# Kernel optimization log

Hardware: AMD Instinct MI355X
Metric: run time of the kernel (lower is better)

Reference implementation:

```python
import jax, jax.numpy as jnp
import numpy as np

B, N, K, D, H = 8, 128, 64, 256, 8  # batch, groups, keys-per-query, k_dim (=h_size), n_head


def setup_inputs() -> dict:
    key = jax.random.key(0)
    kq, kk, kv, kw, kb = jax.random.split(key, 5)
    bound = 1.0 / np.sqrt(D)  # torch nn.Bilinear default init bound
    return {
        "q": jax.random.normal(kq, (B, N, 1, D), jnp.float32),
        "k": jax.random.normal(kk, (B, N, K, D), jnp.float32),
        "v": jax.random.normal(kv, (B, N, K, D), jnp.float32),
        "W": jax.random.uniform(kw, (H, D, D), jnp.float32, -bound, bound),
        "b": jax.random.uniform(kb, (H,), jnp.float32, -bound, bound),
    }


def reference(q, k, v, W, b):
    Bs, Ns, Ks, Ds = k.shape
    Hh = W.shape[0]
    qe = q[:, :, 0, :]  # (B,N,D); torch expands q over K, einsum broadcasts instead
    # nn.Bilinear: scores[b,n,k,h] = q[b,n,:] @ W[h] @ k[b,n,k,:] + b[h]
    scores = jnp.einsum('bnd,hde,bnke->bnkh', qe, W, k) + b  # (B,N,K,H)
    # Faithful to torch's .view(B, N, -1, K): row-major reinterpretation of the
    # trailing (K, H) pair as (H, K) — a dim-mixing reshape, not a transpose.
    attn = scores.reshape(Bs, Ns, Hh, Ks)
    attn = jax.nn.softmax(attn, axis=-1)  # softmax over last dim (dropout p=0)
    # matmul(attn, v) -> (B,N,H,Dv); then sum over the head axis
    output = jnp.einsum('bnhk,bnkd->bnd', attn, v)
    return output, attn
```

## Files before the change

### kernel.cpp

```cpp
#include <hip/hip_runtime.h>
#include <math.h>

namespace {

constexpr int D  = 256;
constexpr int H  = 8;

__global__ __launch_bounds__(256) void qw_kernel(
    const float* __restrict__ q, const float* __restrict__ W,
    float* __restrict__ qW) {
  __shared__ float qT[256][20];
  const int tid = threadIdx.x;
  const int bn0 = blockIdx.x * 16;
  const int h   = blockIdx.y;
  for (int i = 0; i < 16; ++i)
    qT[tid][i] = q[(size_t)(bn0 + i) * D + tid];
  __syncthreads();

  const int r0 = (tid >> 6) << 2;
  const int e0 = (tid & 63) << 2;
  float acc[4][4];
  #pragma unroll
  for (int r = 0; r < 4; ++r)
    #pragma unroll
    for (int e = 0; e < 4; ++e) acc[r][e] = 0.f;

  const float4* W4 = reinterpret_cast<const float4*>(W + (size_t)h * D * D);
  const int ecol = e0 >> 2;
  for (int d = 0; d < D; ++d) {
    float4 qv = *reinterpret_cast<const float4*>(&qT[d][r0]);
    float4 wv = W4[d * 64 + ecol];
    const float qa[4] = {qv.x, qv.y, qv.z, qv.w};
    const float wa[4] = {wv.x, wv.y, wv.z, wv.w};
    #pragma unroll
    for (int r = 0; r < 4; ++r)
      #pragma unroll
      for (int e = 0; e < 4; ++e)
        acc[r][e] += qa[r] * wa[e];
  }
  #pragma unroll
  for (int r = 0; r < 4; ++r) {
    float4 o = make_float4(acc[r][0], acc[r][1], acc[r][2], acc[r][3]);
    *reinterpret_cast<float4*>(&qW[(size_t)(bn0 + r0 + r) * (H * D) + h * D + e0]) = o;
  }
}

__global__ __launch_bounds__(256, 4) void attn_kernel(
    const float* __restrict__ qW, const float* __restrict__ kin,
    const float* __restrict__ vin, const float* __restrict__ bin,
    float* __restrict__ out, float* __restrict__ attn_out) {
  __shared__ float qW_lds[H][260];
  __shared__ float s_lds[512];
  __shared__ float wpart[4][64];
  __shared__ float s_red[4][260];
  const int tid = threadIdx.x;
  const int bn  = blockIdx.x;
  const int wid = tid >> 6;
  const int ln  = tid & 63;

  const float4* v4p = reinterpret_cast<const float4*>(vin) + (size_t)bn * 4096;
  float4 vb0[8];
  #pragma unroll
  for (int j = 0; j < 8; ++j) vb0[j] = v4p[(wid * 16 + j) * 64 + ln];

  const float4* qw4 = reinterpret_cast<const float4*>(qW) + (size_t)bn * 512;
  {
    float4 q0 = qw4[tid];
    float4 q1 = qw4[tid + 256];
    *reinterpret_cast<float4*>(&qW_lds[tid >> 6][(tid & 63) << 2]) = q0;
    *reinterpret_cast<float4*>(&qW_lds[(tid + 256) >> 6][(tid & 63) << 2]) = q1;
  }
  __syncthreads();

  {
    const int krow = tid >> 2;
    const int hp   = tid & 3;
    const float4* k4  = reinterpret_cast<const float4*>(kin) + (size_t)bn * 4096 + krow * 64;
    const float4* a04 = reinterpret_cast<const float4*>(&qW_lds[hp][0]);
    const float4* a14 = reinterpret_cast<const float4*>(&qW_lds[hp + 4][0]);
    float acc0 = bin[hp], acc1 = bin[hp + 4];
    for (int blk = 0; blk < 8; ++blk) {
      float4 kb[8];
      #pragma unroll
      for (int j = 0; j < 8; ++j) kb[j] = k4[blk * 8 + j];
      #pragma unroll
      for (int j = 0; j < 8; ++j) {
        float4 a0 = a04[blk * 8 + j];
        float4 a1 = a14[blk * 8 + j];
        acc0 += a0.x * kb[j].x + a0.y * kb[j].y + a0.z * kb[j].z + a0.w * kb[j].w;
        acc1 += a1.x * kb[j].x + a1.y * kb[j].y + a1.z * kb[j].z + a1.w * kb[j].w;
      }
    }
    s_lds[krow * 8 + hp]     = acc0;
    s_lds[krow * 8 + hp + 4] = acc1;
  }
  __syncthreads();

  float4 vb1[8];
  #pragma unroll
  for (int j = 0; j < 8; ++j) vb1[j] = v4p[(wid * 16 + 8 + j) * 64 + ln];

  {
    float wp = 0.f;
    #pragma unroll
    for (int i = 0; i < 2; ++i) {
      const int c = wid * 2 + i;
      float x = s_lds[c * 64 + ln];
      float m = x;
      #pragma unroll
      for (int off = 32; off; off >>= 1) m = fmaxf(m, __shfl_xor(m, off, 64));
      float e = expf(x - m);
      float s = e;
      #pragma unroll
      for (int off = 32; off; off >>= 1) s += __shfl_xor(s, off, 64);
      float a = e / s;
      attn_out[(size_t)bn * 512 + c * 64 + ln] = a;
      wp += a;
    }
    wpart[wid][ln] = wp;
  }
  __syncthreads();

  {
    float4 acc = make_float4(0.f, 0.f, 0.f, 0.f);
    #pragma unroll
    for (int j = 0; j < 8; ++j) {
      const int kr = wid * 16 + j;
      float w = wpart[0][kr] + wpart[1][kr] + wpart[2][kr] + wpart[3][kr];
      acc.x += w * vb0[j].x; acc.y += w * vb0[j].y;
      acc.z += w * vb0[j].z; acc.w += w * vb0[j].w;
    }
    #pragma unroll
    for (int j = 0; j < 8; ++j) {
      const int kr = wid * 16 + 8 + j;
      float w = wpart[0][kr] + wpart[1][kr] + wpart[2][kr] + wpart[3][kr];
      acc.x += w * vb1[j].x; acc.y += w * vb1[j].y;
      acc.z += w * vb1[j].z; acc.w += w * vb1[j].w;
    }
    *reinterpret_cast<float4*>(&s_red[wid][ln << 2]) = acc;
  }
  __syncthreads();

  out[(size_t)bn * D + tid] =
      s_red[0][tid] + s_red[1][tid] + s_red[2][tid] + s_red[3][tid];
}

}

extern "C" void kernel_launch(void* const* d_in, const int* in_sizes, int n_in,
                              void* d_out, int out_size, void* d_ws, size_t ws_size,
                              hipStream_t stream) {
  const float* q = (const float*)d_in[0];
  const float* k = (const float*)d_in[1];
  const float* v = (const float*)d_in[2];
  const float* W = (const float*)d_in[3];
  const float* b = (const float*)d_in[4];

  float* out  = (float*)d_out;
  float* attn = out + 262144;
  float* qWbuf = (float*)d_ws;

  hipLaunchKernelGGL(qw_kernel, dim3(64, 8), dim3(256), 0, stream, q, W, qWbuf);
  hipLaunchKernelGGL(attn_kernel, dim3(1024), dim3(256), 0, stream, qWbuf, k, v, b, out, attn);
}
```

Baseline: 49.01 us.

## Split fused attention kernel into score/softmax and PV kernels with 2x grid

Replaces the single fused attention kernel with two kernels. The first computes scores and softmax for half of the key rows per block over a 1024x2 grid. The second reads attn back from global memory and computes the weighted sum of v over a 1024x2 grid split by half of D. This exposes more blocks and lowers register pressure (launch bounds go to 8 blocks per SM). The cost is an extra kernel launch, a round trip of attn through global memory, and each score block reloading qW.

```diff
diff --git a/kernel.cpp b/kernel.cpp
--- a/kernel.cpp
+++ b/kernel.cpp
@@ -45,23 +45,16 @@
   }
 }
 
-__global__ __launch_bounds__(256, 4) void attn_kernel(
+__global__ __launch_bounds__(256, 8) void score_kernel(
     const float* __restrict__ qW, const float* __restrict__ kin,
-    const float* __restrict__ vin, const float* __restrict__ bin,
-    float* __restrict__ out, float* __restrict__ attn_out) {
+    const float* __restrict__ bin, float* __restrict__ attn_out) {
   __shared__ float qW_lds[H][260];
-  __shared__ float s_lds[512];
-  __shared__ float wpart[4][64];
-  __shared__ float s_red[4][260];
+  __shared__ float s_lds[256];
   const int tid = threadIdx.x;
   const int bn  = blockIdx.x;
+  const int kh  = blockIdx.y;
   const int wid = tid >> 6;
   const int ln  = tid & 63;
-
-  const float4* v4p = reinterpret_cast<const float4*>(vin) + (size_t)bn * 4096;
-  float4 vb0[8];
-  #pragma unroll
-  for (int j = 0; j < 8; ++j) vb0[j] = v4p[(wid * 16 + j) * 64 + ln];
 
   const float4* qw4 = reinterpret_cast<const float4*>(qW) + (size_t)bn * 512;
   {
@@ -73,76 +66,83 @@
   __syncthreads();
 
   {
-    const int krow = tid >> 2;
-    const int hp   = tid & 3;
-    const float4* k4  = reinterpret_cast<const float4*>(kin) + (size_t)bn * 4096 + krow * 64;
-    const float4* a04 = reinterpret_cast<const float4*>(&qW_lds[hp][0]);
-    const float4* a14 = reinterpret_cast<const float4*>(&qW_lds[hp + 4][0]);
-    float acc0 = bin[hp], acc1 = bin[hp + 4];
+    const int krl = tid >> 3;
+    const int h   = tid & 7;
+    const float4* k4 = reinterpret_cast<const float4*>(kin) +
+                       (size_t)bn * 4096 + (size_t)(kh * 32 + krl) * 64;
+    const float4* a4 = reinterpret_cast<const float4*>(&qW_lds[h][0]);
+    float acc = bin[h];
     for (int blk = 0; blk < 8; ++blk) {
       float4 kb[8];
       #pragma unroll
       for (int j = 0; j < 8; ++j) kb[j] = k4[blk * 8 + j];
       #pragma unroll
       for (int j = 0; j < 8; ++j) {
-        float4 a0 = a04[blk * 8 + j];
-        float4 a1 = a14[blk * 8 + j];
-        acc0 += a0.x * kb[j].x + a0.y * kb[j].y + a0.z * kb[j].z + a0.w * kb[j].w;
-        acc1 += a1.x * kb[j].x + a1.y * kb[j].y + a1.z * kb[j].z + a1.w * kb[j].w;
+        float4 a = a4[blk * 8 + j];
+        acc += a.x * kb[j].x + a.y * kb[j].y + a.z * kb[j].z + a.w * kb[j].w;
       }
     }
-    s_lds[krow * 8 + hp]     = acc0;
-    s_lds[krow * 8 + hp + 4] = acc1;
-  }
-  __syncthreads();
-
-  float4 vb1[8];
-  #pragma unroll
-  for (int j = 0; j < 8; ++j) vb1[j] = v4p[(wid * 16 + 8 + j) * 64 + ln];
-
-  {
-    float wp = 0.f;
-    #pragma unroll
-    for (int i = 0; i < 2; ++i) {
-      const int c = wid * 2 + i;
-      float x = s_lds[c * 64 + ln];
-      float m = x;
-      #pragma unroll
-      for (int off = 32; off; off >>= 1) m = fmaxf(m, __shfl_xor(m, off, 64));
-      float e = expf(x - m);
-      float s = e;
-      #pragma unroll
-      for (int off = 32; off; off >>= 1) s += __shfl_xor(s, off, 64);
-      float a = e / s;
-      attn_out[(size_t)bn * 512 + c * 64 + ln] = a;
-      wp += a;
-    }
-    wpart[wid][ln] = wp;
+    s_lds[krl * 8 + h] = acc;
   }
   __syncthreads();
 
   {
-    float4 acc = make_float4(0.f, 0.f, 0.f, 0.f);
+    float x = s_lds[wid * 64 + ln];
+    float m = x;
     #pragma unroll
-    for (int j = 0; j < 8; ++j) {
-      const int kr = wid * 16 + j;
-      float w = wpart[0][kr] + wpart[1][kr] + wpart[2][kr] + wpart[3][kr];
-      acc.x += w * vb0[j].x; acc.y += w * vb0[j].y;
-      acc.z += w * vb0[j].z; acc.w += w * vb0[j].w;
-    }
+    for (int off = 32; off; off >>= 1) m = fmaxf(m, __shfl_xor(m, off, 64));
+    float e = expf(x - m);
+    float s = e;
     #pragma unroll
-    for (int j = 0; j < 8; ++j) {
-      const int kr = wid * 16 + 8 + j;
-      float w = wpart[0][kr] + wpart[1][kr] + wpart[2][kr] + wpart[3][kr];
-      acc.x += w * vb1[j].x; acc.y += w * vb1[j].y;
-      acc.z += w * vb1[j].z; acc.w += w * vb1[j].w;
-    }
-    *reinterpret_cast<float4*>(&s_red[wid][ln << 2]) = acc;
+    for (int off = 32; off; off >>= 1) s += __shfl_xor(s, off, 64);
+    attn_out[(size_t)bn * 512 + (4 * kh + wid) * 64 + ln] = e / s;
+  }
+}
+
+__global__ __launch_bounds__(256, 8) void pv_kernel(
+    const float* __restrict__ vin, const float* __restrict__ attn_in,
+    float* __restrict__ out) {
+  __shared__ float ws[64];
+  __shared__ float s_red[8][32][4];
+  const int tid = threadIdx.x;
+  const int bn  = blockIdx.x;
+  const int dh  = blockIdx.y;
+
+  if (tid < 64) {
+    const float* ap = attn_in + (size_t)bn * 512 + tid;
+    float w = 0.f;
+    #pragma unroll
+    for (int c = 0; c < 8; ++c) w += ap[c * 64];
+    ws[tid] = w;
   }
   __syncthreads();
 
-  out[(size_t)bn * D + tid] =
-      s_red[0][tid] + s_red[1][tid] + s_red[2][tid] + s_red[3][tid];
+  const int d4 = tid & 31;
+  const int rg = tid >> 5;
+  const float4* v4 = reinterpret_cast<const float4*>(vin) +
+                     (size_t)bn * 4096 + dh * 32;
+  float4 vv[8];
+  #pragma unroll
+  for (int i = 0; i < 8; ++i) vv[i] = v4[(size_t)(rg + i * 8) * 64 + d4];
+  float4 acc = make_float4(0.f, 0.f, 0.f, 0.f);
+  #pragma unroll
+  for (int i = 0; i < 8; ++i) {
+    float w = ws[rg + i * 8];
+    acc.x += w * vv[i].x; acc.y += w * vv[i].y;
+    acc.z += w * vv[i].z; acc.w += w * vv[i].w;
+  }
+  *reinterpret_cast<float4*>(&s_red[rg][d4][0]) = acc;
+  __syncthreads();
+
+  if (tid < 32) {
+    float4 o = make_float4(0.f, 0.f, 0.f, 0.f);
+    #pragma unroll
+    for (int g = 0; g < 8; ++g) {
+      float4 r = *reinterpret_cast<const float4*>(&s_red[g][tid][0]);
+      o.x += r.x; o.y += r.y; o.z += r.z; o.w += r.w;
+    }
+    reinterpret_cast<float4*>(out)[(size_t)bn * 64 + dh * 32 + tid] = o;
+  }
 }
 
 }
@@ -161,5 +161,8 @@
   float* qWbuf = (float*)d_ws;
 
   hipLaunchKernelGGL(qw_kernel, dim3(64, 8), dim3(256), 0, stream, q, W, qWbuf);
-  hipLaunchKernelGGL(attn_kernel, dim3(1024), dim3(256), 0, stream, qWbuf, k, v, b, out, attn);
+  hipLaunchKernelGGL(score_kernel, dim3(1024, 2), dim3(256), 0, stream,
+                     qWbuf, k, b, attn);
+  hipLaunchKernelGGL(pv_kernel, dim3(1024, 2), dim3(256), 0, stream,
+                     v, attn, out);
 }
```

Result: slower. 66.02 us (+34.7%).
